# Optimization experiments

Hardware: AMD Instinct MI355X
Metric: run time of the kernel (lower is better)

## Reference

```python
import jax, jax.numpy as jnp
import numpy as np

B, N, D = 1, 65536, 1024
H = 512
R = 16  # num_regions
C = 2   # num_classes

def _gelu(x):
    return jax.nn.gelu(x, approximate=False)  # torch nn.GELU default is exact erf

def setup_inputs() -> dict:
    key = jax.random.key(0)
    ks = jax.random.split(key, 16)
    s = 0.02
    return {
        "embeddings": jax.random.normal(ks[0], (B, N, D), dtype=jnp.float32),
        # region_encoder: Linear(D,H) + GELU (dropout=0 in eval)
        "W1": jax.random.normal(ks[1], (D, H), dtype=jnp.float32) * s,
        "b1": jnp.zeros((H,), dtype=jnp.float32),
        # region_attention: Linear(H,H//2) -> tanh -> Linear(H//2,1)
        "Wa1": jax.random.normal(ks[2], (H, H // 2), dtype=jnp.float32) * s,
        "ba1": jnp.zeros((H // 2,), dtype=jnp.float32),
        "Wa2": jax.random.normal(ks[3], (H // 2, 1), dtype=jnp.float32) * s,
        "ba2": jnp.zeros((1,), dtype=jnp.float32),
        # slide_encoder: Linear(H,H) + GELU
        "Ws": jax.random.normal(ks[4], (H, H), dtype=jnp.float32) * s,
        "bs": jnp.zeros((H,), dtype=jnp.float32),
        # slide_attention
        "Wsa1": jax.random.normal(ks[5], (H, H // 2), dtype=jnp.float32) * s,
        "bsa1": jnp.zeros((H // 2,), dtype=jnp.float32),
        "Wsa2": jax.random.normal(ks[6], (H // 2, 1), dtype=jnp.float32) * s,
        "bsa2": jnp.zeros((1,), dtype=jnp.float32),
        # classifier: Linear(H,H//2) -> GELU -> Linear(H//2,C)
        "Wc1": jax.random.normal(ks[7], (H, H // 2), dtype=jnp.float32) * s,
        "bc1": jnp.zeros((H // 2,), dtype=jnp.float32),
        "Wc2": jax.random.normal(ks[8], (H // 2, C), dtype=jnp.float32) * s,
        "bc2": jnp.zeros((C,), dtype=jnp.float32),
    }

def reference(embeddings, W1, b1, Wa1, ba1, Wa2, ba2, Ws, bs, Wsa1, bsa1, Wsa2, bsa2, Wc1, bc1, Wc2, bc2):
    b, n, d = embeddings.shape
    m = n // R  # patches per region
    # coords=None path: region_ids[i] = i % R, so region r holds indices r, r+R, ...
    # Equivalent regrouping via reshape+transpose: (B, M, R, D) -> (B, R, M, D)
    x = embeddings.reshape(b, m, R, d).transpose(0, 2, 1, 3)
    # region encoder
    region_emb = _gelu(jnp.einsum('brmd,dh->brmh', x, W1) + b1)  # (B,R,M,H)
    # region attention pooling
    scores = jnp.einsum('brmk,ko->brmo', jnp.tanh(jnp.einsum('brmh,hk->brmk', region_emb, Wa1) + ba1), Wa2) + ba2  # (B,R,M,1)
    attn = jax.nn.softmax(scores, axis=2)
    region_features = jnp.sum(region_emb * attn, axis=2)  # (B,R,H)
    # slide encoder + attention pooling over regions
    slide_emb = _gelu(jnp.einsum('brh,hg->brg', region_features, Ws) + bs)  # (B,R,H)
    sattn = jnp.einsum('brk,ko->bro', jnp.tanh(jnp.einsum('brh,hk->brk', slide_emb, Wsa1) + bsa1), Wsa2) + bsa2  # (B,R,1)
    sweights = jax.nn.softmax(sattn, axis=1)
    slide_rep = jnp.sum(slide_emb * sweights, axis=1)  # (B,H)
    # classifier
    logits = _gelu(slide_rep @ Wc1 + bc1) @ Wc2 + bc2  # (B,C)
    return logits
```

## Files before the change

### kernel.cpp

```cpp
#include <hip/hip_runtime.h>

#define NTOK 65536
#define DIN  1024
#define H    512
#define HH   256
#define NREG 16
#define MPR  4096

__device__ __forceinline__ unsigned short f2bf(float f) {
  unsigned u = __float_as_uint(f);
  u += 0x7fffu + ((u >> 16) & 1u);
  return (unsigned short)(u >> 16);
}
__device__ __forceinline__ float bf2f(unsigned short s) {
  return __uint_as_float(((unsigned)s) << 16);
}
__device__ __forceinline__ float gelu_exact(float x) {
  return 0.5f * x * (1.0f + erff(x * 0.70710678118654752440f));
}
__device__ __forceinline__ unsigned cvt_pk_bf16(float lo, float hi) {
  unsigned r;
  asm("v_cvt_pk_bf16_f32 %0, %1, %2" : "=v"(r) : "v"(lo), "v"(hi));
  return r;
}
__device__ __forceinline__ unsigned short f2bf_hw(float f) {
  unsigned r;
  asm("v_cvt_pk_bf16_f32 %0, %1, %2" : "=v"(r) : "v"(f), "v"(f));
  return (unsigned short)r;
}
__device__ __forceinline__ float fast_tanh(float x) {
  float e = __expf(2.0f * x);
  return 1.0f - 2.0f * __builtin_amdgcn_rcpf(e + 1.0f);
}

typedef __attribute__((ext_vector_type(8))) short shortx8;
typedef __attribute__((ext_vector_type(4))) float floatx4;
typedef __attribute__((ext_vector_type(4))) unsigned int uintx4;

__device__ __forceinline__ void gl_lds16(const void* g, void* l) {
  __builtin_amdgcn_global_load_lds(
      (const __attribute__((address_space(1))) void*)g,
      (__attribute__((address_space(3))) void*)l, 16, 0, 0);
}

__device__ __forceinline__ int swz8(int row, int seg) {
  return (row * 4 + (seg ^ ((row >> 1) & 3))) * 8;
}

__global__ __launch_bounds__(256) void k0_prep(const float* __restrict__ W1,
                                               const float* __restrict__ Wa1,
                                               unsigned short* __restrict__ W1t,
                                               unsigned short* __restrict__ Wa1t) {
  int idx = blockIdx.x * 256 + threadIdx.x;
  if (idx < DIN * H) {
    int n = idx >> 10, k = idx & 1023;
    W1t[idx] = f2bf(W1[k * H + n]);
  } else {
    int i2 = idx - DIN * H;
    int n = i2 >> 9, k = i2 & 511;
    Wa1t[i2] = f2bf(Wa1[k * HH + n]);
  }
}

__global__ __launch_bounds__(512) void k1_gemm1(const float* __restrict__ X,
                                                const unsigned short* __restrict__ W1t,
                                                const float* __restrict__ b1,
                                                unsigned short* __restrict__ Eb) {
  __shared__ __align__(16) short lA[2][128 * 32];
  __shared__ __align__(16) short lB[2][512 * 32];
  const int tid = threadIdx.x;
  const int rowBase = blockIdx.x * 128;
  const int lane = tid & 63;
  const int wave = tid >> 6;
  const int wr = wave >> 2, wc = wave & 3;
  const int l15 = lane & 15, quad = lane >> 4;

  floatx4 acc[4][8] = {};

  const int arow = tid >> 2, aseg = tid & 3;
  const float* aSrc = X + (size_t)(rowBase + arow) * DIN + aseg * 8;
  const int aOff = swz8(arow, aseg);

#pragma unroll
  for (int s = 0; s < 4; s++) {
    int c = tid + s * 512;
    int n = c >> 2;
    int seg = (c & 3) ^ ((n >> 1) & 3);
    gl_lds16(W1t + (size_t)n * DIN + seg * 8, &lB[0][c * 8]);
  }
  {
    const floatx4* src = (const floatx4*)aSrc;
    floatx4 f0 = src[0], f1 = src[1];
    uintx4 u;
    u[0] = cvt_pk_bf16(f0[0], f0[1]);
    u[1] = cvt_pk_bf16(f0[2], f0[3]);
    u[2] = cvt_pk_bf16(f1[0], f1[1]);
    u[3] = cvt_pk_bf16(f1[2], f1[3]);
    *(uintx4*)(&lA[0][aOff]) = u;
  }
  __syncthreads();

#pragma unroll 1
  for (int t = 0; t < 32; ++t) {
    const int cur = t & 1, nxt = cur ^ 1;
    floatx4 f0, f1;
    if (t < 31) {
      const int kb = (t + 1) * 32;
#pragma unroll
      for (int s = 0; s < 4; s++) {
        int c = tid + s * 512;
        int n = c >> 2;
        int seg = (c & 3) ^ ((n >> 1) & 3);
        gl_lds16(W1t + (size_t)n * DIN + kb + seg * 8, &lB[nxt][c * 8]);
      }
      const floatx4* src = (const floatx4*)(aSrc + kb);
      f0 = src[0];
      f1 = src[1];
    }
    shortx8 aF[4], bF[8];
#pragma unroll
    for (int i = 0; i < 4; i++)
      aF[i] = *(const shortx8*)(&lA[cur][swz8(wr * 64 + i * 16 + l15, quad)]);
#pragma unroll
    for (int j = 0; j < 8; j++)
      bF[j] = *(const shortx8*)(&lB[cur][swz8(wc * 128 + j * 16 + l15, quad)]);
#pragma unroll
    for (int i = 0; i < 4; i++)
#pragma unroll
      for (int j = 0; j < 8; j++)
        acc[i][j] = __builtin_amdgcn_mfma_f32_16x16x32_bf16(aF[i], bF[j], acc[i][j], 0, 0, 0);
    if (t < 31) {
      uintx4 u;
      u[0] = cvt_pk_bf16(f0[0], f0[1]);
      u[1] = cvt_pk_bf16(f0[2], f0[3]);
      u[2] = cvt_pk_bf16(f1[0], f1[1]);
      u[3] = cvt_pk_bf16(f1[2], f1[3]);
      *(uintx4*)(&lA[nxt][aOff]) = u;
      __syncthreads();
    }
  }

  const int row0 = rowBase + wr * 64;
#pragma unroll
  for (int j = 0; j < 8; j++) {
    int col = wc * 128 + j * 16 + l15;
    float bias = b1[col];
#pragma unroll
    for (int i = 0; i < 4; i++) {
      int rb = row0 + i * 16 + quad * 4;
#pragma unroll
      for (int v = 0; v < 4; v++) {
        float x = acc[i][j][v] + bias;
        Eb[(size_t)(rb + v) * H + col] = f2bf_hw(gelu_exact(x));
      }
    }
  }
}

__global__ __launch_bounds__(512) void k2_gemm2(const unsigned short* __restrict__ Eb,
                                                const unsigned short* __restrict__ Wa1t,
                                                const float* __restrict__ ba1,
                                                const float* __restrict__ Wa2,
                                                float* __restrict__ scores) {
  __shared__ __align__(16) short lA[2][128 * 32];
  __shared__ __align__(16) short lB[2][256 * 32];
  __shared__ float part[4][128];
  const int tid = threadIdx.x;
  const int rowBase = blockIdx.x * 128;
  const int lane = tid & 63;
  const int wave = tid >> 6;
  const int wr = wave >> 2, wc = wave & 3;
  const int l15 = lane & 15, quad = lane >> 4;

  floatx4 acc[4][4] = {};

  {
    int c = tid;
    int n = c >> 2;
    int seg = (c & 3) ^ ((n >> 1) & 3);
    gl_lds16(Eb + (size_t)(rowBase + n) * H + seg * 8, &lA[0][c * 8]);
  }
#pragma unroll
  for (int s = 0; s < 2; s++) {
    int c = tid + s * 512;
    int n = c >> 2;
    int seg = (c & 3) ^ ((n >> 1) & 3);
    gl_lds16(Wa1t + (size_t)n * H + seg * 8, &lB[0][c * 8]);
  }
  __syncthreads();

#pragma unroll 1
  for (int t = 0; t < 16; ++t) {
    const int cur = t & 1, nxt = cur ^ 1;
    if (t < 15) {
      const int kb = (t + 1) * 32;
      {
        int c = tid;
        int n = c >> 2;
        int seg = (c & 3) ^ ((n >> 1) & 3);
        gl_lds16(Eb + (size_t)(rowBase + n) * H + kb + seg * 8, &lA[nxt][c * 8]);
      }
#pragma unroll
      for (int s = 0; s < 2; s++) {
        int c = tid + s * 512;
        int n = c >> 2;
        int seg = (c & 3) ^ ((n >> 1) & 3);
        gl_lds16(Wa1t + (size_t)n * H + kb + seg * 8, &lB[nxt][c * 8]);
      }
    }
    shortx8 aF[4], bF[4];
#pragma unroll
    for (int i = 0; i < 4; i++)
      aF[i] = *(const shortx8*)(&lA[cur][swz8(wr * 64 + i * 16 + l15, quad)]);
#pragma unroll
    for (int j = 0; j < 4; j++)
      bF[j] = *(const shortx8*)(&lB[cur][swz8(wc * 64 + j * 16 + l15, quad)]);
#pragma unroll
    for (int i = 0; i < 4; i++)
#pragma unroll
      for (int j = 0; j < 4; j++)
        acc[i][j] = __builtin_amdgcn_mfma_f32_16x16x32_bf16(aF[i], bF[j], acc[i][j], 0, 0, 0);
    if (t < 15) __syncthreads();
  }

  float p[4][4];
#pragma unroll
  for (int i = 0; i < 4; i++)
#pragma unroll
    for (int v = 0; v < 4; v++) p[i][v] = 0.0f;
#pragma unroll
  for (int j = 0; j < 4; j++) {
    int col = wc * 64 + j * 16 + l15;
    float bias = ba1[col];
    float wa2 = Wa2[col];
#pragma unroll
    for (int i = 0; i < 4; i++)
#pragma unroll
      for (int v = 0; v < 4; v++)
        p[i][v] += fast_tanh(acc[i][j][v] + bias) * wa2;
  }
#pragma unroll
  for (int i = 0; i < 4; i++)
#pragma unroll
    for (int v = 0; v < 4; v++) {
      float t = p[i][v];
      t += __shfl_xor(t, 1, 16);
      t += __shfl_xor(t, 2, 16);
      t += __shfl_xor(t, 4, 16);
      t += __shfl_xor(t, 8, 16);
      p[i][v] = t;
    }
  if (l15 == 0) {
#pragma unroll
    for (int i = 0; i < 4; i++)
#pragma unroll
      for (int v = 0; v < 4; v++)
        part[wc][wr * 64 + i * 16 + quad * 4 + v] = p[i][v];
  }
  __syncthreads();
  if (tid < 128)
    scores[rowBase + tid] = part[0][tid] + part[1][tid] + part[2][tid] + part[3][tid];
}

__global__ __launch_bounds__(256) void k3a_softmax(const float* __restrict__ scores,
                                                   float* __restrict__ wts) {
  const int r = blockIdx.x, tid = threadIdx.x;
  __shared__ float red[256];
  float m = -1e30f;
  for (int j = tid; j < MPR; j += 256) m = fmaxf(m, scores[r + NREG * j]);
  red[tid] = m;
  __syncthreads();
  for (int s = 128; s > 0; s >>= 1) {
    if (tid < s) red[tid] = fmaxf(red[tid], red[tid + s]);
    __syncthreads();
  }
  float mx = red[0];
  __syncthreads();
  float sum = 0.0f;
  for (int j = tid; j < MPR; j += 256) sum += expf(scores[r + NREG * j] - mx);
  red[tid] = sum;
  __syncthreads();
  for (int s = 128; s > 0; s >>= 1) {
    if (tid < s) red[tid] += red[tid + s];
    __syncthreads();
  }
  float inv = 1.0f / red[0];
  for (int j = tid; j < MPR; j += 256)
    wts[r + NREG * j] = expf(scores[r + NREG * j] - mx) * inv;
}

__global__ __launch_bounds__(256) void k3b_wsum(const unsigned short* __restrict__ Eb,
                                                const float* __restrict__ wts,
                                                float* __restrict__ rf) {
  const int r = blockIdx.y;
  const int mc = blockIdx.x;
  const int tid = threadIdx.x;
  float a0 = 0.0f, a1 = 0.0f;
  for (int j = mc * 128; j < mc * 128 + 128; j++) {
    int n = r + NREG * j;
    float w = wts[n];
    unsigned v = *(const unsigned*)(Eb + (size_t)n * H + tid * 2);
    a0 += w * bf2f((unsigned short)(v & 0xffffu));
    a1 += w * bf2f((unsigned short)(v >> 16));
  }
  atomicAdd(&rf[r * H + tid * 2], a0);
  atomicAdd(&rf[r * H + tid * 2 + 1], a1);
}

__global__ __launch_bounds__(256) void k4a_slide(const float* __restrict__ rf,
                                                 const float* __restrict__ Ws,
                                                 const float* __restrict__ bs,
                                                 float* __restrict__ se) {
  const int r = blockIdx.x, tid = threadIdx.x;
  __shared__ float lrf[H];
  lrf[tid] = rf[r * H + tid];
  lrf[tid + 256] = rf[r * H + tid + 256];
  __syncthreads();
  float a0 = 0.0f, a1 = 0.0f;
  for (int k = 0; k < H; k++) {
    float x = lrf[k];
    a0 += x * Ws[k * H + tid];
    a1 += x * Ws[k * H + tid + 256];
  }
  se[r * H + tid] = gelu_exact(a0 + bs[tid]);
  se[r * H + tid + 256] = gelu_exact(a1 + bs[tid + 256]);
}

__global__ __launch_bounds__(256) void k4b_sscore(const float* __restrict__ se,
                                                  const float* __restrict__ Wsa1,
                                                  const float* __restrict__ bsa1,
                                                  const float* __restrict__ Wsa2,
                                                  const float* __restrict__ bsa2,
                                                  float* __restrict__ ss) {
  const int r = blockIdx.x, tid = threadIdx.x;
  __shared__ float lse[H];
  __shared__ float red[256];
  lse[tid] = se[r * H + tid];
  lse[tid + 256] = se[r * H + tid + 256];
  __syncthreads();
  float a = 0.0f;
  for (int k = 0; k < H; k++) a += lse[k] * Wsa1[k * HH + tid];
  red[tid] = tanhf(a + bsa1[tid]) * Wsa2[tid];
  __syncthreads();
  for (int s = 128; s > 0; s >>= 1) {
    if (tid < s) red[tid] += red[tid + s];
    __syncthreads();
  }
  if (tid == 0) ss[r] = red[0] + bsa2[0];
}

__global__ __launch_bounds__(256) void k4c_final(const float* __restrict__ se,
                                                 const float* __restrict__ ss,
                                                 const float* __restrict__ Wc1,
                                                 const float* __restrict__ bc1,
                                                 const float* __restrict__ Wc2,
                                                 const float* __restrict__ bc2,
                                                 float* __restrict__ out) {
  const int tid = threadIdx.x;
  __shared__ float srep[H];
  __shared__ float r0[256], r1[256];
  float mx = -1e30f;
  for (int i = 0; i < NREG; i++) mx = fmaxf(mx, ss[i]);
  float wv[NREG];
  float den = 0.0f;
  for (int i = 0; i < NREG; i++) { wv[i] = expf(ss[i] - mx); den += wv[i]; }
  float inv = 1.0f / den;
  float s0 = 0.0f, s1 = 0.0f;
  for (int i = 0; i < NREG; i++) {
    float w = wv[i] * inv;
    s0 += w * se[i * H + tid];
    s1 += w * se[i * H + tid + 256];
  }
  srep[tid] = s0;
  srep[tid + 256] = s1;
  __syncthreads();
  float a = 0.0f;
  for (int k = 0; k < H; k++) a += srep[k] * Wc1[k * HH + tid];
  float g = gelu_exact(a + bc1[tid]);
  r0[tid] = g * Wc2[tid * 2];
  r1[tid] = g * Wc2[tid * 2 + 1];
  __syncthreads();
  for (int s = 128; s > 0; s >>= 1) {
    if (tid < s) { r0[tid] += r0[tid + s]; r1[tid] += r1[tid + s]; }
    __syncthreads();
  }
  if (tid == 0) {
    out[0] = r0[0] + bc2[0];
    out[1] = r1[0] + bc2[1];
  }
}

extern "C" void kernel_launch(void* const* d_in, const int* in_sizes, int n_in,
                              void* d_out, int out_size, void* d_ws, size_t ws_size,
                              hipStream_t stream) {
  const float* X    = (const float*)d_in[0];
  const float* W1   = (const float*)d_in[1];
  const float* b1   = (const float*)d_in[2];
  const float* Wa1  = (const float*)d_in[3];
  const float* ba1  = (const float*)d_in[4];
  const float* Wa2  = (const float*)d_in[5];
  const float* Ws   = (const float*)d_in[7];
  const float* bs   = (const float*)d_in[8];
  const float* Wsa1 = (const float*)d_in[9];
  const float* bsa1 = (const float*)d_in[10];
  const float* Wsa2 = (const float*)d_in[11];
  const float* bsa2 = (const float*)d_in[12];
  const float* Wc1  = (const float*)d_in[13];
  const float* bc1  = (const float*)d_in[14];
  const float* Wc2  = (const float*)d_in[15];
  const float* bc2  = (const float*)d_in[16];
  float* out = (float*)d_out;

  char* ws = (char*)d_ws;
  constexpr size_t OFF_W1T  = 0;
  constexpr size_t OFF_WA1T = OFF_W1T + (size_t)H * DIN * 2;
  constexpr size_t OFF_EB   = OFF_WA1T + (size_t)HH * H * 2;
  constexpr size_t OFF_SC   = OFF_EB + (size_t)NTOK * H * 2;
  constexpr size_t OFF_RF   = OFF_SC + (size_t)NTOK * 4;
  constexpr size_t OFF_WT   = OFF_RF + (size_t)NREG * H * 4;
  constexpr size_t OFF_SE   = OFF_WT + (size_t)NTOK * 4;
  constexpr size_t OFF_SS   = OFF_SE + (size_t)NREG * H * 4;

  unsigned short* W1t  = (unsigned short*)(ws + OFF_W1T);
  unsigned short* Wa1t = (unsigned short*)(ws + OFF_WA1T);
  unsigned short* Eb   = (unsigned short*)(ws + OFF_EB);
  float* scores = (float*)(ws + OFF_SC);
  float* rf     = (float*)(ws + OFF_RF);
  float* wts    = (float*)(ws + OFF_WT);
  float* se     = (float*)(ws + OFF_SE);
  float* ssb    = (float*)(ws + OFF_SS);

  hipMemsetAsync(rf, 0, (size_t)NREG * H * 4, stream);

  k0_prep<<<(DIN * H + HH * H) / 256, 256, 0, stream>>>(W1, Wa1, W1t, Wa1t);
  k1_gemm1<<<512, 512, 0, stream>>>(X, W1t, b1, Eb);
  k2_gemm2<<<512, 512, 0, stream>>>(Eb, Wa1t, ba1, Wa2, scores);
  k3a_softmax<<<NREG, 256, 0, stream>>>(scores, wts);
  k3b_wsum<<<dim3(32, NREG), 256, 0, stream>>>(Eb, wts, rf);
  k4a_slide<<<NREG, 256, 0, stream>>>(rf, Ws, bs, se);
  k4b_sscore<<<NREG, 256, 0, stream>>>(se, Wsa1, bsa1, Wsa2, bsa2, ssb);
  k4c_final<<<1, 256, 0, stream>>>(se, ssb, Wc1, bc1, Wc2, bc2, out);
}
```

Baseline: 624.5 us.

## Triple-buffer GEMM K-loops with manual waitcnt barriers and LDS-staged coalesced epilogue

Both GEMM kernels move from double to triple LDS buffering and prefetch two K-tiles ahead. Full __syncthreads are replaced with explicit vmcnt/lgkmcnt waits plus s_barrier, so global loads stay in flight across iterations. The gemm1 epilogue stages GELU outputs through swizzled LDS so Eb is written with 16-byte coalesced stores instead of scattered 2-byte stores, and X is read with nontemporal loads. The extra LDS reduces occupancy, and the hand-counted waitcnts risk races if the counts are wrong.

```diff
diff --git a/kernel.cpp b/kernel.cpp
--- a/kernel.cpp
+++ b/kernel.cpp
@@ -42,6 +42,17 @@
       (const __attribute__((address_space(1))) void*)g,
       (__attribute__((address_space(3))) void*)l, 16, 0, 0);
 }
+
+#define WAITVM(N)                                            \
+  do {                                                       \
+    asm volatile("s_waitcnt vmcnt(" #N ")" ::: "memory");    \
+    __builtin_amdgcn_sched_barrier(0);                       \
+  } while (0)
+#define WAITLGKM0                                            \
+  do {                                                       \
+    asm volatile("s_waitcnt lgkmcnt(0)" ::: "memory");       \
+    __builtin_amdgcn_sched_barrier(0);                       \
+  } while (0)
 
 __device__ __forceinline__ int swz8(int row, int seg) {
   return (row * 4 + (seg ^ ((row >> 1) & 3))) * 8;
@@ -66,8 +77,8 @@
                                                 const unsigned short* __restrict__ W1t,
                                                 const float* __restrict__ b1,
                                                 unsigned short* __restrict__ Eb) {
-  __shared__ __align__(16) short lA[2][128 * 32];
-  __shared__ __align__(16) short lB[2][512 * 32];
+  __shared__ __align__(16) short lA[3][128 * 32];
+  __shared__ __align__(16) short lB[3][512 * 32];
   const int tid = threadIdx.x;
   const int rowBase = blockIdx.x * 128;
   const int lane = tid & 63;
@@ -77,82 +88,134 @@
 
   floatx4 acc[4][8] = {};
 
+  int offA[4], offB[8];
+#pragma unroll
+  for (int i = 0; i < 4; i++) offA[i] = swz8(wr * 64 + i * 16 + l15, quad);
+#pragma unroll
+  for (int j = 0; j < 8; j++) offB[j] = swz8(wc * 128 + j * 16 + l15, quad);
+
   const int arow = tid >> 2, aseg = tid & 3;
-  const float* aSrc = X + (size_t)(rowBase + arow) * DIN + aseg * 8;
+  const float* aPtr = X + (size_t)(rowBase + arow) * DIN + aseg * 8;
   const int aOff = swz8(arow, aseg);
 
+  const unsigned short* bPS[4];
+  int bDst[4];
 #pragma unroll
   for (int s = 0; s < 4; s++) {
     int c = tid + s * 512;
     int n = c >> 2;
     int seg = (c & 3) ^ ((n >> 1) & 3);
-    gl_lds16(W1t + (size_t)n * DIN + seg * 8, &lB[0][c * 8]);
-  }
+    bPS[s] = W1t + (size_t)n * DIN + seg * 8;
+    bDst[s] = c * 8;
+  }
+
   {
-    const floatx4* src = (const floatx4*)aSrc;
-    floatx4 f0 = src[0], f1 = src[1];
+    floatx4 p0 = __builtin_nontemporal_load((const floatx4*)aPtr);
+    floatx4 p1 = __builtin_nontemporal_load((const floatx4*)aPtr + 1);
+    aPtr += 32;
+#pragma unroll
+    for (int s = 0; s < 4; s++) gl_lds16(bPS[s], &lB[0][bDst[s]]);
+#pragma unroll
+    for (int s = 0; s < 4; s++) gl_lds16(bPS[s] + 32, &lB[1][bDst[s]]);
+#pragma unroll
+    for (int s = 0; s < 4; s++) bPS[s] += 64;
     uintx4 u;
-    u[0] = cvt_pk_bf16(f0[0], f0[1]);
-    u[1] = cvt_pk_bf16(f0[2], f0[3]);
-    u[2] = cvt_pk_bf16(f1[0], f1[1]);
-    u[3] = cvt_pk_bf16(f1[2], f1[3]);
+    u[0] = cvt_pk_bf16(p0[0], p0[1]);
+    u[1] = cvt_pk_bf16(p0[2], p0[3]);
+    u[2] = cvt_pk_bf16(p1[0], p1[1]);
+    u[3] = cvt_pk_bf16(p1[2], p1[3]);
     *(uintx4*)(&lA[0][aOff]) = u;
-  }
-  __syncthreads();
+    WAITVM(4);
+    WAITLGKM0;
+    __builtin_amdgcn_s_barrier();
+  }
+
+#define K1_MFMA                                                                  \
+  _Pragma("unroll") for (int i = 0; i < 4; i++)                                  \
+      _Pragma("unroll") for (int j = 0; j < 8; j++)                              \
+          acc[i][j] = __builtin_amdgcn_mfma_f32_16x16x32_bf16(aF[i], bF[j],      \
+                                                              acc[i][j], 0, 0, 0);
+
+#define K1_STEP(CUR, ANB, SB, DO_A, DO_B, AWAIT)                                 \
+  do {                                                                           \
+    shortx8 aF[4], bF[8];                                                        \
+    _Pragma("unroll") for (int i = 0; i < 4; i++)                                \
+        aF[i] = *(const shortx8*)(&lA[CUR][offA[i]]);                            \
+    _Pragma("unroll") for (int j = 0; j < 8; j++)                                \
+        bF[j] = *(const shortx8*)(&lB[CUR][offB[j]]);                            \
+    floatx4 p0, p1;                                                              \
+    if (DO_A) {                                                                  \
+      p0 = __builtin_nontemporal_load((const floatx4*)aPtr);                     \
+      p1 = __builtin_nontemporal_load((const floatx4*)aPtr + 1);                 \
+      aPtr += 32;                                                                \
+    }                                                                            \
+    if (DO_B) {                                                                  \
+      _Pragma("unroll") for (int s = 0; s < 4; s++) {                            \
+        gl_lds16(bPS[s], &lB[SB][bDst[s]]);                                      \
+        bPS[s] += 32;                                                            \
+      }                                                                          \
+    }                                                                            \
+    WAITLGKM0;                                                                   \
+    K1_MFMA;                                                                     \
+    if (DO_A) {                                                                  \
+      AWAIT;                   \
+      uintx4 u;                                                                  \
+      u[0] = cvt_pk_bf16(p0[0], p0[1]);                                          \
+      u[1] = cvt_pk_bf16(p0[2], p0[3]);                                          \
+      u[2] = cvt_pk_bf16(p1[0], p1[1]);                                          \
+      u[3] = cvt_pk_bf16(p1[2], p1[3]);                                          \
+      *(uintx4*)(&lA[ANB][aOff]) = u;                                            \
+    }                                                                            \
+    WAITLGKM0;                                                                   \
+    __builtin_amdgcn_s_barrier();                                                \
+  } while (0)
 
 #pragma unroll 1
-  for (int t = 0; t < 32; ++t) {
-    const int cur = t & 1, nxt = cur ^ 1;
-    floatx4 f0, f1;
-    if (t < 31) {
-      const int kb = (t + 1) * 32;
-#pragma unroll
-      for (int s = 0; s < 4; s++) {
-        int c = tid + s * 512;
-        int n = c >> 2;
-        int seg = (c & 3) ^ ((n >> 1) & 3);
-        gl_lds16(W1t + (size_t)n * DIN + kb + seg * 8, &lB[nxt][c * 8]);
-      }
-      const floatx4* src = (const floatx4*)(aSrc + kb);
-      f0 = src[0];
-      f1 = src[1];
-    }
+  for (int tt = 0; tt < 10; ++tt) {
+    K1_STEP(0, 1, 2, true, true, WAITVM(4));
+    K1_STEP(1, 2, 0, true, true, WAITVM(4));
+    K1_STEP(2, 0, 1, true, true, WAITVM(4));
+  }
+  K1_STEP(0, 1, 2, true, false, WAITVM(0));
+  {
     shortx8 aF[4], bF[8];
 #pragma unroll
-    for (int i = 0; i < 4; i++)
-      aF[i] = *(const shortx8*)(&lA[cur][swz8(wr * 64 + i * 16 + l15, quad)]);
-#pragma unroll
-    for (int j = 0; j < 8; j++)
-      bF[j] = *(const shortx8*)(&lB[cur][swz8(wc * 128 + j * 16 + l15, quad)]);
-#pragma unroll
-    for (int i = 0; i < 4; i++)
+    for (int i = 0; i < 4; i++) aF[i] = *(const shortx8*)(&lA[1][offA[i]]);
+#pragma unroll
+    for (int j = 0; j < 8; j++) bF[j] = *(const shortx8*)(&lB[1][offB[j]]);
+    WAITLGKM0;
+    K1_MFMA;
+  }
+  __builtin_amdgcn_s_barrier();
+
+  short* lE = &lB[0][0];
+  const int row0 = rowBase + wr * 64;
+  float bias[8];
+#pragma unroll
+  for (int j = 0; j < 8; j++) bias[j] = b1[wc * 128 + j * 16 + l15];
+#pragma unroll
+  for (int h = 0; h < 2; h++) {
+    WAITLGKM0;
+#pragma unroll
+    for (int il = 0; il < 2; il++)
 #pragma unroll
       for (int j = 0; j < 8; j++)
-        acc[i][j] = __builtin_amdgcn_mfma_f32_16x16x32_bf16(aF[i], bF[j], acc[i][j], 0, 0, 0);
-    if (t < 31) {
-      uintx4 u;
-      u[0] = cvt_pk_bf16(f0[0], f0[1]);
-      u[1] = cvt_pk_bf16(f0[2], f0[3]);
-      u[2] = cvt_pk_bf16(f1[0], f1[1]);
-      u[3] = cvt_pk_bf16(f1[2], f1[3]);
-      *(uintx4*)(&lA[nxt][aOff]) = u;
-      __syncthreads();
-    }
-  }
-
-  const int row0 = rowBase + wr * 64;
-#pragma unroll
-  for (int j = 0; j < 8; j++) {
-    int col = wc * 128 + j * 16 + l15;
-    float bias = b1[col];
-#pragma unroll
-    for (int i = 0; i < 4; i++) {
-      int rb = row0 + i * 16 + quad * 4;
-#pragma unroll
-      for (int v = 0; v < 4; v++) {
-        float x = acc[i][j][v] + bias;
-        Eb[(size_t)(rb + v) * H + col] = f2bf_hw(gelu_exact(x));
-      }
+#pragma unroll
+        for (int v = 0; v < 4; v++) {
+          int r = il * 16 + quad * 4 + v;
+          int col = j * 16 + l15;
+          float x = acc[2 * h + il][j][v] + bias[j];
+          int chunk = (col >> 3) ^ (r & 7);
+          lE[wave * 4096 + r * 128 + chunk * 8 + (col & 7)] =
+              (short)f2bf_hw(gelu_exact(x));
+        }
+    WAITLGKM0;
+#pragma unroll
+    for (int rr = 0; rr < 8; rr++) {
+      int r = rr * 4 + quad;
+      int chunk = l15 ^ (r & 7);
+      shortx8 val = *(const shortx8*)(&lE[wave * 4096 + r * 128 + chunk * 8]);
+      *(shortx8*)(&Eb[(size_t)(row0 + h * 32 + r) * H + wc * 128 + l15 * 8]) = val;
     }
   }
 }
@@ -162,8 +225,8 @@
                                                 const float* __restrict__ ba1,
                                                 const float* __restrict__ Wa2,
                                                 float* __restrict__ scores) {
-  __shared__ __align__(16) short lA[2][128 * 32];
-  __shared__ __align__(16) short lB[2][256 * 32];
+  __shared__ __align__(16) short lA[3][128 * 32];
+  __shared__ __align__(16) short lB[3][256 * 32];
   __shared__ float part[4][128];
   const int tid = threadIdx.x;
   const int rowBase = blockIdx.x * 128;
@@ -174,53 +237,82 @@
 
   floatx4 acc[4][4] = {};
 
+  int offA[4], offB[4];
+#pragma unroll
+  for (int i = 0; i < 4; i++) offA[i] = swz8(wr * 64 + i * 16 + l15, quad);
+#pragma unroll
+  for (int j = 0; j < 4; j++) offB[j] = swz8(wc * 64 + j * 16 + l15, quad);
+
+  const unsigned short* aPS;
+  int aDst;
   {
-    int c = tid;
-    int n = c >> 2;
+    int c = tid, n = c >> 2;
     int seg = (c & 3) ^ ((n >> 1) & 3);
-    gl_lds16(Eb + (size_t)(rowBase + n) * H + seg * 8, &lA[0][c * 8]);
-  }
+    aPS = Eb + (size_t)(rowBase + n) * H + seg * 8;
+    aDst = c * 8;
+  }
+  const unsigned short* bPS[2];
+  int bDst[2];
 #pragma unroll
   for (int s = 0; s < 2; s++) {
-    int c = tid + s * 512;
-    int n = c >> 2;
+    int c = tid + s * 512, n = c >> 2;
     int seg = (c & 3) ^ ((n >> 1) & 3);
-    gl_lds16(Wa1t + (size_t)n * H + seg * 8, &lB[0][c * 8]);
-  }
-  __syncthreads();
+    bPS[s] = Wa1t + (size_t)n * H + seg * 8;
+    bDst[s] = c * 8;
+  }
+
+  gl_lds16(aPS, &lA[0][aDst]);
+  gl_lds16(bPS[0], &lB[0][bDst[0]]);
+  gl_lds16(bPS[1], &lB[0][bDst[1]]);
+  gl_lds16(aPS + 32, &lA[1][aDst]);
+  gl_lds16(bPS[0] + 32, &lB[1][bDst[0]]);
+  gl_lds16(bPS[1] + 32, &lB[1][bDst[1]]);
+  aPS += 64; bPS[0] += 64; bPS[1] += 64;
+  WAITVM(3);
+  __builtin_amdgcn_s_barrier();
+
+#define K2_MFMA                                                                  \
+  _Pragma("unroll") for (int i = 0; i < 4; i++)                                  \
+      _Pragma("unroll") for (int j = 0; j < 4; j++)                              \
+          acc[i][j] = __builtin_amdgcn_mfma_f32_16x16x32_bf16(aF[i], bF[j],      \
+                                                              acc[i][j], 0, 0, 0);
+
+#define K2_STEP(CUR, SB, DO_B, BW)                                               \
+  do {                                                                           \
+    shortx8 aF[4], bF[4];                                                        \
+    _Pragma("unroll") for (int i = 0; i < 4; i++)                                \
+        aF[i] = *(const shortx8*)(&lA[CUR][offA[i]]);                            \
+    _Pragma("unroll") for (int j = 0; j < 4; j++)                                \
+        bF[j] = *(const shortx8*)(&lB[CUR][offB[j]]);                            \
+    if (DO_B) {                                                                  \
+      gl_lds16(aPS, &lA[SB][aDst]);                                              \
+      gl_lds16(bPS[0], &lB[SB][bDst[0]]);                                        \
+      gl_lds16(bPS[1], &lB[SB][bDst[1]]);                                        \
+      aPS += 32; bPS[0] += 32; bPS[1] += 32;                                     \
+    }                                                                            \
+    WAITLGKM0;                                                                   \
+    K2_MFMA;                                                                     \
+    BW;                                                                          \
+    __builtin_amdgcn_s_barrier();                                                \
+  } while (0)
 
 #pragma unroll 1
-  for (int t = 0; t < 16; ++t) {
-    const int cur = t & 1, nxt = cur ^ 1;
-    if (t < 15) {
-      const int kb = (t + 1) * 32;
-      {
-        int c = tid;
-        int n = c >> 2;
-        int seg = (c & 3) ^ ((n >> 1) & 3);
-        gl_lds16(Eb + (size_t)(rowBase + n) * H + kb + seg * 8, &lA[nxt][c * 8]);
-      }
-#pragma unroll
-      for (int s = 0; s < 2; s++) {
-        int c = tid + s * 512;
-        int n = c >> 2;
-        int seg = (c & 3) ^ ((n >> 1) & 3);
-        gl_lds16(Wa1t + (size_t)n * H + kb + seg * 8, &lB[nxt][c * 8]);
-      }
-    }
+  for (int tt = 0; tt < 4; ++tt) {
+    K2_STEP(0, 2, true, WAITVM(3));
+    K2_STEP(1, 0, true, WAITVM(3));
+    K2_STEP(2, 1, true, WAITVM(3));
+  }
+  K2_STEP(0, 2, true, WAITVM(3));
+  K2_STEP(1, 0, true, WAITVM(3));
+  K2_STEP(2, 1, false, WAITVM(0));
+  {
     shortx8 aF[4], bF[4];
 #pragma unroll
-    for (int i = 0; i < 4; i++)
-      aF[i] = *(const shortx8*)(&lA[cur][swz8(wr * 64 + i * 16 + l15, quad)]);
-#pragma unroll
-    for (int j = 0; j < 4; j++)
-      bF[j] = *(const shortx8*)(&lB[cur][swz8(wc * 64 + j * 16 + l15, quad)]);
-#pragma unroll
-    for (int i = 0; i < 4; i++)
-#pragma unroll
-      for (int j = 0; j < 4; j++)
-        acc[i][j] = __builtin_amdgcn_mfma_f32_16x16x32_bf16(aF[i], bF[j], acc[i][j], 0, 0, 0);
-    if (t < 15) __syncthreads();
+    for (int i = 0; i < 4; i++) aF[i] = *(const shortx8*)(&lA[0][offA[i]]);
+#pragma unroll
+    for (int j = 0; j < 4; j++) bF[j] = *(const shortx8*)(&lB[0][offB[j]]);
+    WAITLGKM0;
+    K2_MFMA;
   }
 
   float p[4][4];
```

Result: no change. 619.8 us (-0.7%).
